# Kernel tuning notes

Measured on AMD Instinct MI355X. Metric: run time of the kernel, lower is better.

Reference implementation:

```python
import jax, jax.numpy as jnp
import numpy as np

DIM = 768
N_HEADS = 12
HEAD_DIM = DIM // N_HEADS  # 64
SEQ = 4096
ROPE_THETA = 10000.0  # local layer (layer_id=1)
WINDOW = 128          # local_attention; mask is distance <= WINDOW // 2


def setup_inputs() -> dict:
    key = jax.random.key(0)
    k1, k2, k3 = jax.random.split(key, 3)
    x = jax.random.normal(k1, (1, SEQ, DIM), dtype=jnp.float32)
    position_ids = jnp.arange(SEQ, dtype=jnp.int64 if jax.config.jax_enable_x64 else jnp.int32).reshape(1, SEQ)
    wqkv = jax.random.normal(k2, (3 * DIM, DIM), dtype=jnp.float32) * 0.02
    wo = jax.random.normal(k3, (DIM, DIM), dtype=jnp.float32) * 0.02
    return {"x": x, "position_ids": position_ids, "wqkv": wqkv, "wo": wo}


def _rope_cos_sin(position_ids):
    # inv_freq over even dims, freqs duplicated to full head_dim
    inv_freq = 1.0 / (ROPE_THETA ** (jnp.arange(0, HEAD_DIM, 2, dtype=jnp.float32) / HEAD_DIM))
    pos = position_ids.reshape(-1).astype(jnp.float32)           # [S]
    freqs = pos[:, None] * inv_freq[None, :]                      # [S, hd/2]
    freqs = jnp.concatenate([freqs, freqs], axis=-1)              # [S, hd]
    return jnp.cos(freqs)[None, None], jnp.sin(freqs)[None, None]  # [1,1,S,hd]


def _rotate_half(t):
    h = t.shape[-1] // 2
    return jnp.concatenate([-t[..., h:], t[..., :h]], axis=-1)


def reference(x, position_ids, wqkv, wo):
    bsz, seq_len, _ = x.shape
    qkv = jnp.einsum("bsd,ed->bse", x, wqkv)                      # [B,S,3*dim]
    qkv = qkv.reshape(bsz, seq_len, 3, N_HEADS, HEAD_DIM)
    qkv = jnp.transpose(qkv, (0, 3, 2, 1, 4))                      # [B,H,3,S,hd]
    q, k, v = qkv[:, :, 0], qkv[:, :, 1], qkv[:, :, 2]             # [B,H,S,hd]

    cos, sin = _rope_cos_sin(position_ids)
    q = q * cos + _rotate_half(q) * sin
    k = k * cos + _rotate_half(k) * sin

    scale = HEAD_DIM ** -0.5
    scores = jnp.einsum("bhqd,bhkd->bhqk", q, k) * scale           # [B,H,S,S]

    # sliding-window mask: |i - j| <= WINDOW // 2
    idx = jnp.arange(seq_len)
    dist = jnp.abs(idx[None, :] - idx[:, None])                    # [S,S]
    window_mask = dist <= (WINDOW // 2)
    scores = jnp.where(window_mask[None, None], scores, -jnp.inf)

    attn = jax.nn.softmax(scores, axis=-1)
    out = jnp.einsum("bhqk,bhkd->bhqd", attn, v)                   # [B,H,S,hd]
    out = jnp.transpose(out, (0, 2, 1, 3)).reshape(bsz, seq_len, DIM)
    out = jnp.einsum("bsd,ed->bse", out, wo)
    return out
```

## Files before the change

kernel.cpp:

```cpp
#include <hip/hip_runtime.h>
#include <math.h>

#define SEQ 4096
#define DIM 768
#define NH 12
#define HD 64
#define QKV_N 2304
#define HALF_WIN 64
#define QBLK 64

typedef __attribute__((ext_vector_type(8))) short bf16x8;
typedef __attribute__((ext_vector_type(4))) float floatx4;

__device__ __forceinline__ unsigned short f2bf(float f) {
    unsigned u = __float_as_uint(f);
    unsigned r = (u + 0x7fffu + ((u >> 16) & 1u)) >> 16;
    return (unsigned short)r;
}

__device__ __forceinline__ void gld16(const void* g, void* l) {
    __builtin_amdgcn_global_load_lds(
        (const __attribute__((address_space(1))) unsigned*)g,
        (__attribute__((address_space(3))) unsigned*)l, 16, 0, 0);
}

__device__ __forceinline__ void fast_sc(float x, float* s, float* c) {
    float r = x * 0.15915494309189535f;
    r = r - floorf(r);
    *s = __builtin_amdgcn_sinf(r);
    *c = __builtin_amdgcn_cosf(r);
}

__global__ __launch_bounds__(256) void cast3_bf16(const float* __restrict__ x,
                                                  const float* __restrict__ wqkv,
                                                  const float* __restrict__ wo,
                                                  unsigned short* __restrict__ dst,
                                                  int nx4, int nw4, int ntot4) {
    int i = blockIdx.x * 256 + threadIdx.x;
    if (i >= ntot4) return;
    const float4* src;
    int off;
    if (i < nx4)            { src = (const float4*)x;    off = i; }
    else if (i < nx4 + nw4) { src = (const float4*)wqkv; off = i - nx4; }
    else                    { src = (const float4*)wo;   off = i - nx4 - nw4; }
    float4 v = src[off];
    ushort4 r;
    r.x = f2bf(v.x); r.y = f2bf(v.y); r.z = f2bf(v.z); r.w = f2bf(v.w);
    *(ushort4*)(dst + (size_t)i * 4) = r;
}

__global__ __launch_bounds__(256, 3) void gemm_qkv_rope(const unsigned short* __restrict__ A,
                                                        const unsigned short* __restrict__ B,
                                                        unsigned short* __restrict__ qr,
                                                        unsigned short* __restrict__ kr,
                                                        unsigned short* __restrict__ vt) {
    __shared__ __align__(16) short smem[24576];
    const int t  = threadIdx.x;
    const int wv = t >> 6, ln = t & 63;
    const int o    = blockIdx.y * 18 + blockIdx.x;
    const int xcd  = o & 7;
    const int j    = o >> 3;
    const int bm0  = (xcd * 8 + (j & 7)) * 64;
    const int bn0  = (j >> 3) * 128;
    const int lrow = ln >> 3;
    const int lu   = ln & 7;
    const int frow = ln & 15;
    const int q    = ln >> 4;
    const int K = DIM;
    const int wn = wv;
    const int nbase = (wn >> 1) * 64 + (wn & 1) * 16;

    const unsigned short* gptr[6];
    int loff[6];
#pragma unroll
    for (int i = 0; i < 6; i++) {
        int idx = wv * 6 + i;
        int c   = (idx < 8) ? idx : idx - 8;
        int row = c * 8 + lrow;
        int g   = (lu ^ (row & 7)) << 3;
        if (idx < 8) {
            gptr[i] = A + (size_t)(bm0 + row) * K + g;
            loff[i] = c * 512;
        } else {
            gptr[i] = B + (size_t)(bn0 + row) * K + g;
            loff[i] = 4096 + c * 512;
        }
    }

    floatx4 acc[4][2];
#pragma unroll
    for (int i = 0; i < 4; i++)
#pragma unroll
        for (int j2 = 0; j2 < 2; j2++) acc[i][j2] = (floatx4){0.f, 0.f, 0.f, 0.f};

#pragma unroll
    for (int i = 0; i < 6; i++) gld16(gptr[i], (void*)(smem + loff[i]));
    __syncthreads();

    int cur = 0;
    for (int it = 0; it < 12; it++) {
        if (it + 1 < 12) {
            int nb = cur ^ 1;
            int k0n = (it + 1) * 64;
#pragma unroll
            for (int i = 0; i < 6; i++)
                gld16(gptr[i] + k0n, (void*)(smem + nb * 12288 + loff[i]));
        }
        short* As = smem + cur * 12288;
        short* Bs = As + 4096;
#pragma unroll
        for (int ks = 0; ks < 2; ks++) {
            bf16x8 af[4], bfr[2];
#pragma unroll
            for (int mt = 0; mt < 4; mt++) {
                int ra = mt * 16 + frow;
                af[mt] = *(const bf16x8*)&As[ra * 64 + (((ks * 4 + q) ^ (ra & 7)) << 3)];
            }
#pragma unroll
            for (int nt = 0; nt < 2; nt++) {
                int rb = nbase + nt * 32 + frow;
                bfr[nt] = *(const bf16x8*)&Bs[rb * 64 + (((ks * 4 + q) ^ (rb & 7)) << 3)];
            }
#pragma unroll
            for (int mt = 0; mt < 4; mt++)
#pragma unroll
                for (int nt = 0; nt < 2; nt++)
                    acc[mt][nt] = __builtin_amdgcn_mfma_f32_16x16x32_bf16(
                        af[mt], bfr[nt], acc[mt][nt], 0, 0, 0);
        }
        __syncthreads();
        cur ^= 1;
    }

    const int cn = frow;
    const int part = (bn0 >= 1536) ? 2 : (bn0 >= 768 ? 1 : 0);

    if (part < 2) {
        const int di = (wn & 1) * 16 + cn;
        const int h  = (bn0 - part * 768 + (wn >> 1) * 64) >> 6;
        unsigned short* dst = (part == 0 ? qr : kr) + (size_t)h * SEQ * HD;
        const float invf = exp2f(-(float)di * 0.4152410118609203f);
#pragma unroll
        for (int mt = 0; mt < 4; mt++) {
            const int sbase = bm0 + mt * 16 + q * 4;
#pragma unroll
            for (int r = 0; r < 4; r++) {
                float ss = (float)(sbase + r);
                float sn, cs;
                fast_sc(ss * invf, &sn, &cs);
                float lo = acc[mt][0][r] * cs - acc[mt][1][r] * sn;
                float hi = acc[mt][1][r] * cs + acc[mt][0][r] * sn;
                unsigned short* p = dst + (size_t)(sbase + r) * HD + di;
                p[0]  = f2bf(lo);
                p[32] = f2bf(hi);
            }
        }
    } else {
        short* vstage = smem;
#pragma unroll
        for (int nt = 0; nt < 2; nt++) {
#pragma unroll
            for (int mt = 0; mt < 4; mt++) {
                int d    = nbase + nt * 32 + cn;
                int sloc = mt * 16 + q * 4;
                ushort4 pk;
                pk.x = f2bf(acc[mt][nt][0]);
                pk.y = f2bf(acc[mt][nt][1]);
                pk.z = f2bf(acc[mt][nt][2]);
                pk.w = f2bf(acc[mt][nt][3]);
                *(ushort4*)&vstage[d * 72 + sloc] = pk;
            }
        }
        __syncthreads();
        const int dr = t >> 1, su = (t & 1) * 32;
        uint4 v0 = *(const uint4*)&vstage[dr * 72 + su];
        uint4 v1 = *(const uint4*)&vstage[dr * 72 + su + 8];
        uint4 v2 = *(const uint4*)&vstage[dr * 72 + su + 16];
        uint4 v3 = *(const uint4*)&vstage[dr * 72 + su + 24];
        unsigned short* vp = vt + (size_t)(bn0 - 1536 + dr) * SEQ + bm0 + su;
        *(uint4*)(vp)      = v0;
        *(uint4*)(vp + 8)  = v1;
        *(uint4*)(vp + 16) = v2;
        *(uint4*)(vp + 24) = v3;
    }
}

__global__ __launch_bounds__(256) void gemm_out(const unsigned short* __restrict__ A,
                                                const unsigned short* __restrict__ B,
                                                float* __restrict__ C,
                                                int M, int N, int K) {
    __shared__ __align__(16) short smem[16384];
    const int t  = threadIdx.x;
    const int wv = t >> 6, ln = t & 63;
    const int wm = wv >> 1, wn = wv & 1;
    const int o   = blockIdx.y * 12 + blockIdx.x;
    const int xcd = o & 7;
    const int j   = o >> 3;
    const int bm0 = (xcd * 8 + (j & 7)) * 64;
    const int bn0 = (j >> 3) * 64;
    const int lrow = ln >> 3;
    const int lu   = ln & 7;
    const int frow = ln & 15;
    const int q    = ln >> 4;

    const unsigned short* gptr[4];
    int loff[4];
#pragma unroll
    for (int i = 0; i < 4; i++) {
        int idx = wv * 4 + i;
        int c   = (idx < 8) ? idx : idx - 8;
        int row = c * 8 + lrow;
        int g   = (lu ^ (row & 7)) << 3;
        if (idx < 8) {
            gptr[i] = A + (size_t)(bm0 + row) * K + g;
            loff[i] = c * 512;
        } else {
            gptr[i] = B + (size_t)(bn0 + row) * K + g;
            loff[i] = 4096 + c * 512;
        }
    }

    floatx4 acc[2][2];
#pragma unroll
    for (int i = 0; i < 2; i++)
#pragma unroll
        for (int j2 = 0; j2 < 2; j2++) acc[i][j2] = (floatx4){0.f, 0.f, 0.f, 0.f};

#pragma unroll
    for (int i = 0; i < 4; i++) gld16(gptr[i], (void*)(smem + loff[i]));
    __syncthreads();

    int cur = 0;
    const int NIT = K / 64;
    for (int it = 0; it < NIT; it++) {
        if (it + 1 < NIT) {
            int nb = cur ^ 1;
            int k0n = (it + 1) * 64;
#pragma unroll
            for (int i = 0; i < 4; i++)
                gld16(gptr[i] + k0n, (void*)(smem + nb * 8192 + loff[i]));
        }
        short* As = smem + cur * 8192;
        short* Bs = As + 4096;
#pragma unroll
        for (int ks = 0; ks < 2; ks++) {
            bf16x8 af[2], bfr[2];
#pragma unroll
            for (int mt = 0; mt < 2; mt++) {
                int ra = wm * 32 + mt * 16 + frow;
                af[mt] = *(const bf16x8*)&As[ra * 64 + (((ks * 4 + q) ^ (ra & 7)) << 3)];
            }
#pragma unroll
            for (int nt = 0; nt < 2; nt++) {
                int rb = wn * 32 + nt * 16 + frow;
                bfr[nt] = *(const bf16x8*)&Bs[rb * 64 + (((ks * 4 + q) ^ (rb & 7)) << 3)];
            }
#pragma unroll
            for (int mt = 0; mt < 2; mt++)
#pragma unroll
                for (int nt = 0; nt < 2; nt++)
                    acc[mt][nt] = __builtin_amdgcn_mfma_f32_16x16x32_bf16(
                        af[mt], bfr[nt], acc[mt][nt], 0, 0, 0);
        }
        __syncthreads();
        cur ^= 1;
    }

    const int cn = ln & 15;
    const int rb4 = (ln >> 4) * 4;
#pragma unroll
    for (int mt = 0; mt < 2; mt++) {
#pragma unroll
        for (int nt = 0; nt < 2; nt++) {
            floatx4 v = acc[mt][nt];
            float* cp = C + (size_t)(bm0 + wm * 32 + mt * 16 + rb4) * N +
                        bn0 + wn * 32 + nt * 16 + cn;
#pragma unroll
            for (int r = 0; r < 4; r++) cp[(size_t)r * N] = v[r];
        }
    }
}

__global__ __launch_bounds__(256) void attn_mfma(const unsigned short* __restrict__ Q,
                                                 const unsigned short* __restrict__ K,
                                                 const unsigned short* __restrict__ Vt,
                                                 unsigned short* __restrict__ Out) {
    __shared__ __align__(16) short lds[20480];
    short* Pb = lds + 16384;
    const int t  = threadIdx.x;
    const int wv = t >> 6, ln = t & 63;
    const int o = blockIdx.y * 12 + blockIdx.x;
    const int L = (o & 7) * 96 + (o >> 3);
    const int h  = L % 12;
    const int qs = (L / 12) * QBLK;
    const int frow = ln & 15, qd = ln >> 4;
    const int rl = ln >> 3, uu = ln & 7;
    const unsigned short* Qh = Q + (size_t)h * SEQ * HD;
    const unsigned short* Kh = K + (size_t)h * SEQ * HD;
    const unsigned short* Vh = Vt + (size_t)h * HD * SEQ;

    const unsigned short* qp = Qh + (size_t)(qs + wv * 16 + frow) * HD;
    bf16x8 af0 = *(const bf16x8*)(qp + qd * 8);
    bf16x8 af1 = *(const bf16x8*)(qp + (qd + 4) * 8);

    floatx4 accO[4];
#pragma unroll
    for (int i = 0; i < 4; i++) accO[i] = (floatx4){0.f, 0.f, 0.f, 0.f};
    float m_r[4] = {-1e30f, -1e30f, -1e30f, -1e30f};
    float l_r[4] = {0.f, 0.f, 0.f, 0.f};

    const int qlo = wv * 16;
    const int srow0 = wv * 16 + rl;
    const int srow1 = srow0 + 8;
    const int sg0 = uu ^ ((srow0 + (srow0 >> 3)) & 7);
    const int sg1 = uu ^ ((srow1 + (srow1 >> 3)) & 7);

    {
        const int kb0 = qs - 64;
        const int kbc = kb0 < 0 ? 0 : (kb0 > SEQ - 64 ? SEQ - 64 : kb0);
        gld16(Kh + (size_t)(kbc + srow0) * HD + sg0 * 8, (void*)(lds + (wv * 16) * 64));
        gld16(Kh + (size_t)(kbc + srow1) * HD + sg1 * 8, (void*)(lds + (wv * 16 + 8) * 64));
        gld16(Vh + (size_t)srow0 * SEQ + kbc + sg0 * 8, (void*)(lds + 4096 + (wv * 16) * 64));
        gld16(Vh + (size_t)srow1 * SEQ + kbc + sg1 * 8, (void*)(lds + 4096 + (wv * 16 + 8) * 64));
    }
    __syncthreads();

    int cur = 0;
    for (int c = 0; c < 3; c++) {
        if (c + 1 < 3) {
            const int kb1 = qs - 64 + (c + 1) * 64;
            const int kbc1 = kb1 < 0 ? 0 : (kb1 > SEQ - 64 ? SEQ - 64 : kb1);
            short* nb = lds + (cur ^ 1) * 8192;
            gld16(Kh + (size_t)(kbc1 + srow0) * HD + sg0 * 8, (void*)(nb + (wv * 16) * 64));
            gld16(Kh + (size_t)(kbc1 + srow1) * HD + sg1 * 8, (void*)(nb + (wv * 16 + 8) * 64));
            gld16(Vh + (size_t)srow0 * SEQ + kbc1 + sg0 * 8, (void*)(nb + 4096 + (wv * 16) * 64));
            gld16(Vh + (size_t)srow1 * SEQ + kbc1 + sg1 * 8, (void*)(nb + 4096 + (wv * 16 + 8) * 64));
        }
        short* Ks  = lds + cur * 8192;
        short* Vts = Ks + 4096;
        const int kb = qs - 64 + c * 64;

        const int klo0 = c * 64 - 64;
        bool live_kt[4];
        bool any_live = false;
#pragma unroll
        for (int kt = 0; kt < 4; kt++) {
            int d0 = qlo - (klo0 + kt * 16);
            live_kt[kt] = (d0 <= 64) && (d0 >= -64);
            any_live = any_live || live_kt[kt];
        }

        if (any_live) {
            float sv[4][4];
            float cm[4] = {-1e30f, -1e30f, -1e30f, -1e30f};
#pragma unroll
            for (int kt = 0; kt < 4; kt++) {
                if (live_kt[kt]) {
                    int brow = kt * 16 + frow;
                    int bz = (brow + (brow >> 3)) & 7;
                    bf16x8 b0 = *(const bf16x8*)&Ks[brow * 64 + ((qd ^ bz) << 3)];
                    bf16x8 b1 = *(const bf16x8*)&Ks[brow * 64 + (((qd + 4) ^ bz) << 3)];
                    floatx4 z = (floatx4){0.f, 0.f, 0.f, 0.f};
                    z = __builtin_amdgcn_mfma_f32_16x16x32_bf16(af0, b0, z, 0, 0, 0);
                    z = __builtin_amdgcn_mfma_f32_16x16x32_bf16(af1, b1, z, 0, 0, 0);
                    int gk = kb + kt * 16 + frow;
#pragma unroll
                    for (int r = 0; r < 4; r++) {
                        int gq = qs + wv * 16 + qd * 4 + r;
                        int dd = gq - gk;
                        bool valid = (gk >= 0) && (gk < SEQ) &&
                                     (dd <= HALF_WIN) && (dd >= -HALF_WIN);
                        float x = valid ? z[r] * 0.125f : -1e30f;
                        sv[kt][r] = x;
                        cm[r] = fmaxf(cm[r], x);
                    }
                } else {
#pragma unroll
                    for (int r = 0; r < 4; r++) sv[kt][r] = -1e30f;
                }
            }
#pragma unroll
            for (int off = 1; off < 16; off <<= 1)
#pragma unroll
                for (int r = 0; r < 4; r++)
                    cm[r] = fmaxf(cm[r], __shfl_xor(cm[r], off, 64));
            float al[4], ls[4];
#pragma unroll
            for (int r = 0; r < 4; r++) {
                float mn = fmaxf(m_r[r], cm[r]);
                al[r] = __expf(m_r[r] - mn);
                m_r[r] = mn;
                ls[r] = 0.f;
            }
            const int qrb = wv * 16 + qd * 4;
#pragma unroll
            for (int kt = 0; kt < 4; kt++) {
                int klocal = kt * 16 + frow;
                int ku = klocal >> 3;
                if (live_kt[kt]) {
#pragma unroll
                    for (int r = 0; r < 4; r++) {
                        float p = (sv[kt][r] > -1e29f) ? __expf(sv[kt][r] - m_r[r]) : 0.f;
                        ls[r] += p;
                        int qrow = qrb + r;
                        int pz = (qrow + (qrow >> 3)) & 7;
                        Pb[qrow * 64 + ((ku ^ pz) << 3) + (klocal & 7)] = (short)f2bf(p);
                    }
                } else {
#pragma unroll
                    for (int r = 0; r < 4; r++) {
                        int qrow = qrb + r;
                        int pz = (qrow + (qrow >> 3)) & 7;
                        Pb[qrow * 64 + ((ku ^ pz) << 3) + (klocal & 7)] = 0;
                    }
                }
            }
#pragma unroll
            for (int off = 1; off < 16; off <<= 1)
#pragma unroll
                for (int r = 0; r < 4; r++) ls[r] += __shfl_xor(ls[r], off, 64);
#pragma unroll
            for (int r = 0; r < 4; r++) l_r[r] = l_r[r] * al[r] + ls[r];
#pragma unroll
            for (int dt = 0; dt < 4; dt++)
#pragma unroll
                for (int r = 0; r < 4; r++) accO[dt][r] *= al[r];

            const int prow = wv * 16 + frow;
            const int pz2 = (prow + (prow >> 3)) & 7;
            bf16x8 pa0 = *(const bf16x8*)&Pb[prow * 64 + ((qd ^ pz2) << 3)];
            bf16x8 pa1 = *(const bf16x8*)&Pb[prow * 64 + (((qd + 4) ^ pz2) << 3)];
#pragma unroll
            for (int dt = 0; dt < 4; dt++) {
                int vrow = dt * 16 + frow;
                int vz = (vrow + (vrow >> 3)) & 7;
                bf16x8 v0 = *(const bf16x8*)&Vts[vrow * 64 + ((qd ^ vz) << 3)];
                bf16x8 v1 = *(const bf16x8*)&Vts[vrow * 64 + (((qd + 4) ^ vz) << 3)];
                accO[dt] = __builtin_amdgcn_mfma_f32_16x16x32_bf16(pa0, v0, accO[dt], 0, 0, 0);
                accO[dt] = __builtin_amdgcn_mfma_f32_16x16x32_bf16(pa1, v1, accO[dt], 0, 0, 0);
            }
        }
        __syncthreads();
        cur ^= 1;
    }

    short* Ob = lds;
    float linv[4];
#pragma unroll
    for (int r = 0; r < 4; r++) linv[r] = 1.0f / l_r[r];
#pragma unroll
    for (int dt = 0; dt < 4; dt++)
#pragma unroll
        for (int r = 0; r < 4; r++) {
            int qrow = wv * 16 + qd * 4 + r;
            int dcol = dt * 16 + frow;
            Ob[qrow * 72 + dcol] = (short)f2bf(accO[dt][r] * linv[r]);
        }
    __syncthreads();
    const int orow = t >> 2, og = (t & 3) * 16;
    uint4 a = *(const uint4*)&Ob[orow * 72 + og];
    uint4 b = *(const uint4*)&Ob[orow * 72 + og + 8];
    unsigned short* op = Out + (size_t)(qs + orow) * DIM + h * HD + og;
    *(uint4*)(op)     = a;
    *(uint4*)(op + 8) = b;
}

extern "C" void kernel_launch(void* const* d_in, const int* in_sizes, int n_in,
                              void* d_out, int out_size, void* d_ws, size_t ws_size,
                              hipStream_t stream) {
    const float* x    = (const float*)d_in[0];
    const float* wqkv = (const float*)d_in[2];
    const float* wo   = (const float*)d_in[3];
    float* out = (float*)d_out;

    unsigned short* q_r  = (unsigned short*)d_ws;
    unsigned short* k_r  = q_r + (size_t)NH * SEQ * HD;
    unsigned short* v_t  = k_r + (size_t)NH * SEQ * HD;
    unsigned short* x_bf = v_t + (size_t)NH * SEQ * HD;
    unsigned short* wqkv_bf = x_bf + (size_t)SEQ * DIM;
    unsigned short* wo_bf   = wqkv_bf + (size_t)QKV_N * DIM;
    unsigned short* attn_bf = wo_bf + (size_t)DIM * DIM;

    const int nx4 = SEQ * DIM / 4;
    const int nw4 = QKV_N * DIM / 4;
    const int no4 = DIM * DIM / 4;
    const int ntot4 = nx4 + nw4 + no4;

    cast3_bf16<<<dim3((ntot4 + 255) / 256), 256, 0, stream>>>(
        x, wqkv, wo, x_bf, nx4, nw4, ntot4);
    gemm_qkv_rope<<<dim3(QKV_N / 128, SEQ / 64), 256, 0, stream>>>(
        x_bf, wqkv_bf, q_r, k_r, v_t);
    attn_mfma<<<dim3(NH, SEQ / QBLK), 256, 0, stream>>>(
        q_r, k_r, v_t, attn_bf);
    gemm_out<<<dim3(DIM / 64, SEQ / 64), 256, 0, stream>>>(
        attn_bf, wo_bf, out, SEQ, DIM, DIM);
}
```

Measured before the change: 119.6 us.

## Replace online softmax with two-pass softmax over whole window in attention

The attention kernel now computes all three key-chunk score tiles into registers first, takes a single row max, and then runs exp and the PV MFMAs. This removes the per-chunk online rescaling of the accumulator, the running max/sum bookkeeping and the repeated shuffle reductions. All three V chunks are loaded into LDS up front while K stays double-buffered, and fully in-window 16-key tiles skip per-element mask checks. The cost is more LDS per block (48KB instead of 40KB) and more live registers for the stored scores, which may lower occupancy.

```diff
diff --git a/kernel.cpp b/kernel.cpp
--- a/kernel.cpp
+++ b/kernel.cpp
@@ -285,8 +285,8 @@
                                                  const unsigned short* __restrict__ K,
                                                  const unsigned short* __restrict__ Vt,
                                                  unsigned short* __restrict__ Out) {
-    __shared__ __align__(16) short lds[20480];
-    short* Pb = lds + 16384;
+    __shared__ __align__(16) short lds[24576];
+    short* Pb = lds + 20480;
     const int t  = threadIdx.x;
     const int wv = t >> 6, ln = t & 63;
     const int o = blockIdx.y * 12 + blockIdx.x;
@@ -303,12 +303,6 @@
     bf16x8 af0 = *(const bf16x8*)(qp + qd * 8);
     bf16x8 af1 = *(const bf16x8*)(qp + (qd + 4) * 8);
 
-    floatx4 accO[4];
-#pragma unroll
-    for (int i = 0; i < 4; i++) accO[i] = (floatx4){0.f, 0.f, 0.f, 0.f};
-    float m_r[4] = {-1e30f, -1e30f, -1e30f, -1e30f};
-    float l_r[4] = {0.f, 0.f, 0.f, 0.f};
-
     const int qlo = wv * 16;
     const int srow0 = wv * 16 + rl;
     const int srow1 = srow0 + 8;
@@ -320,49 +314,49 @@
         const int kbc = kb0 < 0 ? 0 : (kb0 > SEQ - 64 ? SEQ - 64 : kb0);
         gld16(Kh + (size_t)(kbc + srow0) * HD + sg0 * 8, (void*)(lds + (wv * 16) * 64));
         gld16(Kh + (size_t)(kbc + srow1) * HD + sg1 * 8, (void*)(lds + (wv * 16 + 8) * 64));
-        gld16(Vh + (size_t)srow0 * SEQ + kbc + sg0 * 8, (void*)(lds + 4096 + (wv * 16) * 64));
-        gld16(Vh + (size_t)srow1 * SEQ + kbc + sg1 * 8, (void*)(lds + 4096 + (wv * 16 + 8) * 64));
+    }
+#pragma unroll
+    for (int c = 0; c < 3; c++) {
+        const int kb = qs - 64 + c * 64;
+        const int kbc = kb < 0 ? 0 : (kb > SEQ - 64 ? SEQ - 64 : kb);
+        short* vs = lds + 8192 + c * 4096;
+        gld16(Vh + (size_t)srow0 * SEQ + kbc + sg0 * 8, (void*)(vs + (wv * 16) * 64));
+        gld16(Vh + (size_t)srow1 * SEQ + kbc + sg1 * 8, (void*)(vs + (wv * 16 + 8) * 64));
     }
     __syncthreads();
 
-    int cur = 0;
+    float sv[3][4][4];
+#pragma unroll
     for (int c = 0; c < 3; c++) {
         if (c + 1 < 3) {
             const int kb1 = qs - 64 + (c + 1) * 64;
             const int kbc1 = kb1 < 0 ? 0 : (kb1 > SEQ - 64 ? SEQ - 64 : kb1);
-            short* nb = lds + (cur ^ 1) * 8192;
+            short* nb = lds + ((c + 1) & 1) * 4096;
             gld16(Kh + (size_t)(kbc1 + srow0) * HD + sg0 * 8, (void*)(nb + (wv * 16) * 64));
             gld16(Kh + (size_t)(kbc1 + srow1) * HD + sg1 * 8, (void*)(nb + (wv * 16 + 8) * 64));
-            gld16(Vh + (size_t)srow0 * SEQ + kbc1 + sg0 * 8, (void*)(nb + 4096 + (wv * 16) * 64));
-            gld16(Vh + (size_t)srow1 * SEQ + kbc1 + sg1 * 8, (void*)(nb + 4096 + (wv * 16 + 8) * 64));
-        }
-        short* Ks  = lds + cur * 8192;
-        short* Vts = Ks + 4096;
+        }
+        short* Ks = lds + (c & 1) * 4096;
         const int kb = qs - 64 + c * 64;
-
-        const int klo0 = c * 64 - 64;
-        bool live_kt[4];
-        bool any_live = false;
 #pragma unroll
         for (int kt = 0; kt < 4; kt++) {
-            int d0 = qlo - (klo0 + kt * 16);
-            live_kt[kt] = (d0 <= 64) && (d0 >= -64);
-            any_live = any_live || live_kt[kt];
-        }
-
-        if (any_live) {
-            float sv[4][4];
-            float cm[4] = {-1e30f, -1e30f, -1e30f, -1e30f};
-#pragma unroll
-            for (int kt = 0; kt < 4; kt++) {
-                if (live_kt[kt]) {
-                    int brow = kt * 16 + frow;
-                    int bz = (brow + (brow >> 3)) & 7;
-                    bf16x8 b0 = *(const bf16x8*)&Ks[brow * 64 + ((qd ^ bz) << 3)];
-                    bf16x8 b1 = *(const bf16x8*)&Ks[brow * 64 + (((qd + 4) ^ bz) << 3)];
-                    floatx4 z = (floatx4){0.f, 0.f, 0.f, 0.f};
-                    z = __builtin_amdgcn_mfma_f32_16x16x32_bf16(af0, b0, z, 0, 0, 0);
-                    z = __builtin_amdgcn_mfma_f32_16x16x32_bf16(af1, b1, z, 0, 0, 0);
+            const int klo = c * 64 - 64 + kt * 16;
+            const int d0  = qlo - klo;
+            const int gk0 = qs + klo;
+            const bool dead = (d0 > 64) || (d0 < -64) || (gk0 + 16 <= 0) || (gk0 >= SEQ);
+            if (!dead) {
+                int brow = kt * 16 + frow;
+                int bz = (brow + (brow >> 3)) & 7;
+                bf16x8 b0 = *(const bf16x8*)&Ks[brow * 64 + ((qd ^ bz) << 3)];
+                bf16x8 b1 = *(const bf16x8*)&Ks[brow * 64 + (((qd + 4) ^ bz) << 3)];
+                floatx4 z = (floatx4){0.f, 0.f, 0.f, 0.f};
+                z = __builtin_amdgcn_mfma_f32_16x16x32_bf16(af0, b0, z, 0, 0, 0);
+                z = __builtin_amdgcn_mfma_f32_16x16x32_bf16(af1, b1, z, 0, 0, 0);
+                const bool full = (d0 <= 48) && (d0 >= -48) &&
+                                  (gk0 >= 0) && (gk0 + 16 <= SEQ);
+                if (full) {
+#pragma unroll
+                    for (int r = 0; r < 4; r++) sv[c][kt][r] = z[r] * 0.125f;
+                } else {
                     int gk = kb + kt * 16 + frow;
 #pragma unroll
                     for (int r = 0; r < 4; r++) {
@@ -370,66 +364,70 @@
                         int dd = gq - gk;
                         bool valid = (gk >= 0) && (gk < SEQ) &&
                                      (dd <= HALF_WIN) && (dd >= -HALF_WIN);
-                        float x = valid ? z[r] * 0.125f : -1e30f;
-                        sv[kt][r] = x;
-                        cm[r] = fmaxf(cm[r], x);
-                    }
-                } else {
-#pragma unroll
-                    for (int r = 0; r < 4; r++) sv[kt][r] = -1e30f;
-                }
-            }
-#pragma unroll
-            for (int off = 1; off < 16; off <<= 1)
-#pragma unroll
-                for (int r = 0; r < 4; r++)
-                    cm[r] = fmaxf(cm[r], __shfl_xor(cm[r], off, 64));
-            float al[4], ls[4];
-#pragma unroll
-            for (int r = 0; r < 4; r++) {
-                float mn = fmaxf(m_r[r], cm[r]);
-                al[r] = __expf(m_r[r] - mn);
-                m_r[r] = mn;
-                ls[r] = 0.f;
-            }
-            const int qrb = wv * 16 + qd * 4;
-#pragma unroll
-            for (int kt = 0; kt < 4; kt++) {
-                int klocal = kt * 16 + frow;
-                int ku = klocal >> 3;
-                if (live_kt[kt]) {
-#pragma unroll
-                    for (int r = 0; r < 4; r++) {
-                        float p = (sv[kt][r] > -1e29f) ? __expf(sv[kt][r] - m_r[r]) : 0.f;
-                        ls[r] += p;
-                        int qrow = qrb + r;
-                        int pz = (qrow + (qrow >> 3)) & 7;
-                        Pb[qrow * 64 + ((ku ^ pz) << 3) + (klocal & 7)] = (short)f2bf(p);
-                    }
-                } else {
-#pragma unroll
-                    for (int r = 0; r < 4; r++) {
-                        int qrow = qrb + r;
-                        int pz = (qrow + (qrow >> 3)) & 7;
-                        Pb[qrow * 64 + ((ku ^ pz) << 3) + (klocal & 7)] = 0;
+                        sv[c][kt][r] = valid ? z[r] * 0.125f : -1e30f;
                     }
                 }
-            }
-#pragma unroll
-            for (int off = 1; off < 16; off <<= 1)
-#pragma unroll
-                for (int r = 0; r < 4; r++) ls[r] += __shfl_xor(ls[r], off, 64);
-#pragma unroll
-            for (int r = 0; r < 4; r++) l_r[r] = l_r[r] * al[r] + ls[r];
-#pragma unroll
-            for (int dt = 0; dt < 4; dt++)
-#pragma unroll
-                for (int r = 0; r < 4; r++) accO[dt][r] *= al[r];
-
+            } else {
+#pragma unroll
+                for (int r = 0; r < 4; r++) sv[c][kt][r] = -1e30f;
+            }
+        }
+        __syncthreads();
+    }
+
+    float cm[4] = {-1e30f, -1e30f, -1e30f, -1e30f};
+#pragma unroll
+    for (int c = 0; c < 3; c++)
+#pragma unroll
+        for (int kt = 0; kt < 4; kt++)
+#pragma unroll
+            for (int r = 0; r < 4; r++) cm[r] = fmaxf(cm[r], sv[c][kt][r]);
+#pragma unroll
+    for (int off = 1; off < 16; off <<= 1)
+#pragma unroll
+        for (int r = 0; r < 4; r++) cm[r] = fmaxf(cm[r], __shfl_xor(cm[r], off, 64));
+
+    floatx4 accO[4];
+#pragma unroll
+    for (int i = 0; i < 4; i++) accO[i] = (floatx4){0.f, 0.f, 0.f, 0.f};
+    float ls[4] = {0.f, 0.f, 0.f, 0.f};
+    const int qrb = wv * 16 + qd * 4;
+#pragma unroll
+    for (int c = 0; c < 3; c++) {
+        bool anyl = false;
+#pragma unroll
+        for (int kt = 0; kt < 4; kt++) {
+            const int klo = c * 64 - 64 + kt * 16;
+            const int d0  = qlo - klo;
+            const int gk0 = qs + klo;
+            const bool dead = (d0 > 64) || (d0 < -64) || (gk0 + 16 <= 0) || (gk0 >= SEQ);
+            const int klocal = kt * 16 + frow;
+            const int ku = klocal >> 3;
+            if (!dead) {
+                anyl = true;
+#pragma unroll
+                for (int r = 0; r < 4; r++) {
+                    float p = __expf(sv[c][kt][r] - cm[r]);
+                    ls[r] += p;
+                    int qrow = qrb + r;
+                    int pz = (qrow + (qrow >> 3)) & 7;
+                    Pb[qrow * 64 + ((ku ^ pz) << 3) + (klocal & 7)] = (short)f2bf(p);
+                }
+            } else {
+#pragma unroll
+                for (int r = 0; r < 4; r++) {
+                    int qrow = qrb + r;
+                    int pz = (qrow + (qrow >> 3)) & 7;
+                    Pb[qrow * 64 + ((ku ^ pz) << 3) + (klocal & 7)] = 0;
+                }
+            }
+        }
+        if (anyl) {
             const int prow = wv * 16 + frow;
             const int pz2 = (prow + (prow >> 3)) & 7;
             bf16x8 pa0 = *(const bf16x8*)&Pb[prow * 64 + ((qd ^ pz2) << 3)];
             bf16x8 pa1 = *(const bf16x8*)&Pb[prow * 64 + (((qd + 4) ^ pz2) << 3)];
+            short* Vts = lds + 8192 + c * 4096;
 #pragma unroll
             for (int dt = 0; dt < 4; dt++) {
                 int vrow = dt * 16 + frow;
@@ -440,14 +438,16 @@
                 accO[dt] = __builtin_amdgcn_mfma_f32_16x16x32_bf16(pa1, v1, accO[dt], 0, 0, 0);
             }
         }
-        __syncthreads();
-        cur ^= 1;
-    }
+    }
+#pragma unroll
+    for (int off = 1; off < 16; off <<= 1)
+#pragma unroll
+        for (int r = 0; r < 4; r++) ls[r] += __shfl_xor(ls[r], off, 64);
 
     short* Ob = lds;
     float linv[4];
 #pragma unroll
-    for (int r = 0; r < 4; r++) linv[r] = 1.0f / l_r[r];
+    for (int r = 0; r < 4; r++) linv[r] = 1.0f / ls[r];
 #pragma unroll
     for (int dt = 0; dt < 4; dt++)
 #pragma unroll
```

Result: no change. 119.8 us (+0.2%).
